# Kernel optimization log

Measured on AMD Instinct MI355X. Metric: run time of the kernel, lower is better.

The kernel has to match this reference:

```python
import jax, jax.numpy as jnp
import numpy as np

ALPHABET = 4
SKETCH_DIM = 128
SUBSEQ = 8
SEQ_LEN = 8192


def setup_inputs() -> dict:
    key = jax.random.key(0)
    k1, k2, k3 = jax.random.split(key, 3)
    sequence = jax.random.randint(k1, (SEQ_LEN,), 0, ALPHABET, dtype=jnp.int32)
    # stacked Linear(A, d, bias=False) weights, xavier-uniform-ish init
    limit = float(np.sqrt(6.0 / (ALPHABET + SKETCH_DIM)))
    hash_weights = jax.random.uniform(k2, (SUBSEQ, SKETCH_DIM, ALPHABET),
                                      minval=-limit, maxval=limit, dtype=jnp.float32)
    sign_weights = jax.random.normal(k3, (SUBSEQ, ALPHABET), dtype=jnp.float32)
    return {"sequence": sequence, "hash_weights": hash_weights, "sign_weights": sign_weights}


def _sketch(sequence, hash_weights, sign_weights):
    P, d, A = hash_weights.shape
    seq_len = sequence.shape[0]
    # circulant gather indices: roll(src, s)[j] == src[(j - s) % d]
    j = jnp.arange(d)
    idx = (j[:, None] - j[None, :]) % d  # [d(out), d(shift)]
    p_ids = jnp.arange(1, P + 1)
    z_num = p_ids.astype(jnp.float32)

    Tp0 = jnp.zeros((P + 1, d), jnp.float32).at[0, 0].set(1.0)
    Tm0 = jnp.zeros((P + 1, d), jnp.float32)

    def step(carry, xs):
        Tp, Tm = carry
        i, c = xs
        valid = (c >= 0) & (c < A)
        cc = jnp.clip(c, 0, A - 1)
        hv = hash_weights[:, :, cc]                      # [P, d]
        probs = jax.nn.softmax(hv, axis=1)               # [P, d]
        sign = jax.nn.sigmoid(sign_weights[:, cc])       # [P]
        denom = (i + 1).astype(jnp.float32)
        z = (z_num / denom)[:, None]                     # [P, 1]
        gate = ((p_ids <= i + 1) & valid)[:, None]       # [P, 1]
        # soft circular shift: sum_s probs[s] * roll(source, s)
        convP = jnp.einsum('pjs,ps->pj', Tp[:P][:, idx], probs)
        convM = jnp.einsum('pjs,ps->pj', Tm[:P][:, idx], probs)
        newP = jnp.where(gate, (1.0 - z) * Tp[1:] + z * sign[:, None] * convP, Tp[1:])
        newM = jnp.where(gate, (1.0 - z) * Tm[1:] + z * (1.0 - sign[:, None]) * convM, Tm[1:])
        return (Tp.at[1:].set(newP), Tm.at[1:].set(newM)), None

    (Tp, Tm), _ = jax.lax.scan(step, (Tp0, Tm0), (jnp.arange(seq_len), sequence))
    return Tp[P] - Tm[P]


def reference(sequence, hash_weights, sign_weights):
    return _sketch(sequence, hash_weights, sign_weights)
```

## Files before the change

kernel.cpp:

```cpp
#include <hip/hip_runtime.h>
#include <math.h>

#define DDIM 128
#define NSEQ 8192
#define SUB 16
#define SEG 64
#define NSEGB 128
#define COMB 16
#define NCOMB 8
#define NTRI 45

#define TRI(L,q) ((L)*((L)+1)/2 + (q))

#define OFF_PHAT 0
#define OFF_AB   32768
#define OFF_MSEG 557056
#define OFF_MG2  6455296

__device__ __forceinline__ void loadG(const float2* __restrict__ p, int fq,
                                      float (&R)[NTRI], float (&I)[NTRI]) {
#pragma unroll
  for (int e = 0; e < NTRI; ++e) {
    float2 t = p[e*128 + fq];
    R[e] = t.x; I[e] = t.y;
  }
}

__device__ __forceinline__ void matvec(const float (&GR)[NTRI], const float (&GI)[NTRI],
                                       float (&vr)[9], float (&vi)[9]) {
#pragma unroll
  for (int L = 8; L >= 0; --L) {
    float sr = 0.f, si = 0.f;
#pragma unroll
    for (int q = 0; q <= L; ++q) {
      float xr = vr[q], xi = vi[q];
      sr += GR[TRI(L,q)]*xr - GI[TRI(L,q)]*xi;
      si += GR[TRI(L,q)]*xi + GI[TRI(L,q)]*xr;
    }
    vr[L] = sr; vi[L] = si;
  }
}

__device__ __forceinline__ void matmul(const float (&BR)[NTRI], const float (&BI)[NTRI],
                                       float (&Ar)[NTRI], float (&Ai)[NTRI]) {
#pragma unroll
  for (int L = 8; L >= 0; --L) {
    float tr[9], ti[9];
#pragma unroll
    for (int q = 0; q <= L; ++q) {
      float sr = 0.f, si = 0.f;
#pragma unroll
      for (int r = q; r <= L; ++r) {
        float br = BR[TRI(L,r)], bi = BI[TRI(L,r)];
        float ar = Ar[TRI(r,q)], ai = Ai[TRI(r,q)];
        sr += br*ar - bi*ai;
        si += br*ai + bi*ar;
      }
      tr[q] = sr; ti[q] = si;
    }
#pragma unroll
    for (int q = 0; q <= L; ++q) { Ar[TRI(L,q)] = tr[q]; Ai[TRI(L,q)] = ti[q]; }
  }
}

__global__ __launch_bounds__(128)
void sk_setup(const int* __restrict__ seq,
              const float* __restrict__ hw,
              const float* __restrict__ sw,
              float2* __restrict__ phat,
              float2* __restrict__ ab)
{
  const int tid = threadIdx.x;
  const int bid = blockIdx.x;

  if (bid < 32) {
    __shared__ float probs[128];
    __shared__ float ct[128], st[128];
    __shared__ float red[4];
    const int r = bid, p = r >> 2, c = r & 3;
    const int wave = tid >> 6, lane = tid & 63;

    float h = hw[p*512 + tid*4 + c];
    float mx = h;
    #pragma unroll
    for (int off = 1; off < 64; off <<= 1) mx = fmaxf(mx, __shfl_xor(mx, off));
    if (lane == 0) red[wave] = mx;
    __syncthreads();
    mx = fmaxf(red[0], red[1]);
    float e = expf(h - mx);
    float s = e;
    #pragma unroll
    for (int off = 1; off < 64; off <<= 1) s += __shfl_xor(s, off);
    if (lane == 0) red[2 + wave] = s;
    float th = 6.28318530717958647692f * (float)tid / 128.0f;
    ct[tid] = cosf(th); st[tid] = sinf(th);
    __syncthreads();
    s = red[2] + red[3];
    probs[tid] = e / s;
    __syncthreads();

    float ar = 0.f, ai = 0.f;
    for (int j = 0; j < 128; ++j) {
      float pv = probs[j];
      int w = (j * tid) & 127;
      ar += pv * ct[w];
      ai -= pv * st[w];
    }
    phat[(c*8 + p)*128 + tid] = make_float2(ar, ai);
  } else {
    const int total = NSEQ * 8;
    for (int n = (bid - 32)*128 + tid; n < total; n += 64*128) {
      const int i = n >> 3, Lm1 = n & 7, L = Lm1 + 1;
      int cc0 = seq[i];
      bool valid = (cc0 >= 0) && (cc0 < 4);
      int cc = min(max(cc0, 0), 3);
      bool gate = valid && (L <= i + 1);
      float z  = (float)L / (float)(i + 1);
      float sg = 1.0f / (1.0f + expf(-sw[Lm1*4 + cc]));
      float a = gate ? (1.0f - z) : 1.0f;
      float b = gate ? (z * sg) : 0.0f;
      ab[n] = make_float2(a, b);
    }
  }
}

__global__ __launch_bounds__(512, 1)
void sk_seg(const int* __restrict__ seq,
            const float2* __restrict__ phat_g,
            const float2* __restrict__ ab_g,
            float2* __restrict__ mseg)
{
  __shared__ float2 phS[4096];
  __shared__ float2 abS[SEG*8];
  __shared__ int    chS[SEG];
  __shared__ float2 tb[2][NTRI*128];
  const int tid = threadIdx.x;
  const int u   = tid >> 7, fq = tid & 127;
  const int m   = blockIdx.x;

  {
    const float4* src = (const float4*)phat_g;
    float4* dst = (float4*)phS;
    for (int i = tid; i < 2048; i += 512) dst[i] = src[i];
  }
  for (int i = tid; i < SEG*8; i += 512) abS[i] = ab_g[m*SEG*8 + i];
  if (tid < SEG) chS[tid] = seq[m*SEG + tid];
  __syncthreads();

  float Mr[NTRI], Mi[NTRI];
  #pragma unroll
  for (int e = 0; e < NTRI; ++e) { Mr[e] = 0.f; Mi[e] = 0.f; }
  #pragma unroll
  for (int L = 0; L <= 8; ++L) Mr[TRI(L,L)] = 1.0f;

  const int t0 = u * SUB;
  for (int t = 0; t < SUB; ++t) {
    const int ts = t0 + t;
    const int c  = chS[ts];
    #pragma unroll
    for (int L = 8; L >= 1; --L) {
      float2 abv = abS[ts*8 + (L-1)];
      float2 Pv  = phS[(c*8 + (L-1))*128 + fq];
      const float a = abv.x;
      const float bPr = abv.y * Pv.x, bPi = abv.y * Pv.y;
      #pragma unroll
      for (int q = 0; q < L; ++q) {
        float xr = Mr[TRI(L-1,q)], xi = Mi[TRI(L-1,q)];
        Mr[TRI(L,q)] = a*Mr[TRI(L,q)] + (bPr*xr - bPi*xi);
        Mi[TRI(L,q)] = a*Mi[TRI(L,q)] + (bPr*xi + bPi*xr);
      }
      Mr[TRI(L,L)] *= a;
      Mi[TRI(L,L)] *= a;
    }
  }

  if (u == 1 || u == 3) {
    float2* b = tb[u >> 1];
    #pragma unroll
    for (int e = 0; e < NTRI; ++e) b[e*128 + fq] = make_float2(Mr[e], Mi[e]);
  }
  __syncthreads();
  if (u == 0 || u == 2) {
    const float2* b = tb[u >> 1];
    float Br[NTRI], Bi[NTRI];
    #pragma unroll
    for (int e = 0; e < NTRI; ++e) { float2 t = b[e*128 + fq]; Br[e] = t.x; Bi[e] = t.y; }
    matmul(Br, Bi, Mr, Mi);
  }
  __syncthreads();
  if (u == 2) {
    #pragma unroll
    for (int e = 0; e < NTRI; ++e) tb[1][e*128 + fq] = make_float2(Mr[e], Mi[e]);
  }
  __syncthreads();
  if (u == 0) {
    float Br[NTRI], Bi[NTRI];
    #pragma unroll
    for (int e = 0; e < NTRI; ++e) { float2 t = tb[1][e*128 + fq]; Br[e] = t.x; Bi[e] = t.y; }
    matmul(Br, Bi, Mr, Mi);
    #pragma unroll
    for (int e = 0; e < NTRI; ++e)
      mseg[((size_t)m*NTRI + e)*128 + fq] = make_float2(Mr[e], Mi[e]);
  }
}

__global__ __launch_bounds__(512, 1)
void sk_comb1(const float2* __restrict__ mseg, float2* __restrict__ mg2)
{
  __shared__ float2 tb[2][NTRI*128];
  const int tid = threadIdx.x;
  const int u   = tid >> 7, fq = tid & 127;
  const int g   = blockIdx.x;
  const float2* bp = mseg + (size_t)(g*COMB + u*4) * NTRI * 128;

  float Ar[NTRI], Ai[NTRI], Br[NTRI], Bi[NTRI];
  loadG(bp, fq, Ar, Ai);
  loadG(bp + (size_t)1*NTRI*128, fq, Br, Bi);  matmul(Br, Bi, Ar, Ai);
  loadG(bp + (size_t)2*NTRI*128, fq, Br, Bi);  matmul(Br, Bi, Ar, Ai);
  loadG(bp + (size_t)3*NTRI*128, fq, Br, Bi);  matmul(Br, Bi, Ar, Ai);

  if (u == 1 || u == 3) {
    float2* b = tb[u >> 1];
    #pragma unroll
    for (int e = 0; e < NTRI; ++e) b[e*128 + fq] = make_float2(Ar[e], Ai[e]);
  }
  __syncthreads();
  if (u == 0 || u == 2) {
    const float2* b = tb[u >> 1];
    #pragma unroll
    for (int e = 0; e < NTRI; ++e) { float2 t = b[e*128 + fq]; Br[e] = t.x; Bi[e] = t.y; }
    matmul(Br, Bi, Ar, Ai);
  }
  __syncthreads();
  if (u == 2) {
    #pragma unroll
    for (int e = 0; e < NTRI; ++e) tb[1][e*128 + fq] = make_float2(Ar[e], Ai[e]);
  }
  __syncthreads();
  if (u == 0) {
    #pragma unroll
    for (int e = 0; e < NTRI; ++e) { float2 t = tb[1][e*128 + fq]; Br[e] = t.x; Bi[e] = t.y; }
    matmul(Br, Bi, Ar, Ai);
    #pragma unroll
    for (int e = 0; e < NTRI; ++e)
      mg2[((size_t)g*NTRI + e)*128 + fq] = make_float2(Ar[e], Ai[e]);
  }
}

__global__ __launch_bounds__(512, 1)
void sk_fin(const float2* __restrict__ mg2, float* __restrict__ out)
{
  __shared__ float2 vS[9*128];
  __shared__ float Ur[128], Ui[128];
  __shared__ float ct[128], st[128];
  const int tid = threadIdx.x;
  const int u   = tid >> 7, fq = tid & 127;

  float Ar[NTRI], Ai[NTRI], Br[NTRI], Bi[NTRI];
  loadG(mg2 + (size_t)(2*u)  *NTRI*128, fq, Ar, Ai);
  loadG(mg2 + (size_t)(2*u+1)*NTRI*128, fq, Br, Bi);

  if (tid < 128) {
    float th = 6.28318530717958647692f * (float)tid / 128.0f;
    ct[tid] = cosf(th); st[tid] = sinf(th);
  }

  float vr[9], vi[9];
  if (u == 0) {
    #pragma unroll
    for (int L = 0; L <= 8; ++L) { vr[L] = Ar[TRI(L,0)]; vi[L] = Ai[TRI(L,0)]; }
    matvec(Br, Bi, vr, vi);
    #pragma unroll
    for (int L = 0; L <= 8; ++L) vS[L*128 + fq] = make_float2(vr[L], vi[L]);
  }
  __syncthreads();
  for (int uu = 1; uu < 4; ++uu) {
    if (u == uu) {
      #pragma unroll
      for (int L = 0; L <= 8; ++L) { float2 t = vS[L*128 + fq]; vr[L] = t.x; vi[L] = t.y; }
      matvec(Ar, Ai, vr, vi);
      matvec(Br, Bi, vr, vi);
      #pragma unroll
      for (int L = 0; L <= 8; ++L) vS[L*128 + fq] = make_float2(vr[L], vi[L]);
    }
    __syncthreads();
  }

  if (tid < 128) {
    float2 uv = vS[8*128 + tid];
    Ur[tid] = uv.x; Ui[tid] = uv.y;
  }
  __syncthreads();

  if (tid < 128) {
    float acc = 0.f;
    for (int k = 0; k < 128; ++k) {
      int w = (tid * k) & 127;
      acc += Ur[k]*ct[w] - Ui[k]*st[w];
    }
    out[tid] = acc * (1.0f/128.0f);
  }
}

extern "C" void kernel_launch(void* const* d_in, const int* in_sizes, int n_in,
                              void* d_out, int out_size, void* d_ws, size_t ws_size,
                              hipStream_t stream)
{
  const int*   seq = (const int*)d_in[0];
  const float* hw  = (const float*)d_in[1];
  const float* sw  = (const float*)d_in[2];

  char* base = (char*)d_ws;
  float2* phat = (float2*)(base + OFF_PHAT);
  float2* ab   = (float2*)(base + OFF_AB);
  float2* mseg = (float2*)(base + OFF_MSEG);
  float2* mg2  = (float2*)(base + OFF_MG2);

  sk_setup<<<96, 128, 0, stream>>>(seq, hw, sw, phat, ab);
  sk_seg<<<NSEGB, 512, 0, stream>>>(seq, phat, ab, mseg);
  sk_comb1<<<NCOMB, 512, 0, stream>>>(mseg, mg2);
  sk_fin<<<1, 512, 0, stream>>>(mg2, (float*)d_out);
}
```

Before: 140.0 us.

## Split segment combination into two parallel tree levels and widen final chain

```diff
diff --git a/kernel.cpp b/kernel.cpp
--- a/kernel.cpp
+++ b/kernel.cpp
@@ -6,8 +6,6 @@
 #define SUB 16
 #define SEG 64
 #define NSEGB 128
-#define COMB 16
-#define NCOMB 8
 #define NTRI 45
 
 #define TRI(L,q) ((L)*((L)+1)/2 + (q))
@@ -15,7 +13,8 @@
 #define OFF_PHAT 0
 #define OFF_AB   32768
 #define OFF_MSEG 557056
-#define OFF_MG2  6455296
+#define OFF_MT1  6455296
+#define OFF_MT2  7929856
 
 __device__ __forceinline__ void loadG(const float2* __restrict__ p, int fq,
                                       float (&R)[NTRI], float (&I)[NTRI]) {
@@ -24,6 +23,12 @@
     float2 t = p[e*128 + fq];
     R[e] = t.x; I[e] = t.y;
   }
+}
+
+__device__ __forceinline__ void publish(float2* __restrict__ b, int fq,
+                                        const float (&R)[NTRI], const float (&I)[NTRI]) {
+#pragma unroll
+  for (int e = 0; e < NTRI; ++e) b[e*128 + fq] = make_float2(R[e], I[e]);
 }
 
 __device__ __forceinline__ void matvec(const float (&GR)[NTRI], const float (&GI)[NTRI],
@@ -41,20 +46,25 @@
   }
 }
 
-__device__ __forceinline__ void matmul(const float (&BR)[NTRI], const float (&BI)[NTRI],
-                                       float (&Ar)[NTRI], float (&Ai)[NTRI]) {
+__device__ __forceinline__ void matmulL(const float2* __restrict__ b, int fq,
+                                        float (&Ar)[NTRI], float (&Ai)[NTRI]) {
 #pragma unroll
   for (int L = 8; L >= 0; --L) {
+    float Br_[9], Bi_[9];
+#pragma unroll
+    for (int r = 0; r <= L; ++r) {
+      float2 t = b[TRI(L,r)*128 + fq];
+      Br_[r] = t.x; Bi_[r] = t.y;
+    }
     float tr[9], ti[9];
 #pragma unroll
     for (int q = 0; q <= L; ++q) {
       float sr = 0.f, si = 0.f;
 #pragma unroll
       for (int r = q; r <= L; ++r) {
-        float br = BR[TRI(L,r)], bi = BI[TRI(L,r)];
         float ar = Ar[TRI(r,q)], ai = Ai[TRI(r,q)];
-        sr += br*ar - bi*ai;
-        si += br*ai + bi*ar;
+        sr += Br_[r]*ar - Bi_[r]*ai;
+        si += Br_[r]*ai + Bi_[r]*ar;
       }
       tr[q] = sr; ti[q] = si;
     }
@@ -124,7 +134,7 @@
   }
 }
 
-__global__ __launch_bounds__(512, 1)
+__global__ __launch_bounds__(512)
 void sk_seg(const int* __restrict__ seq,
             const float2* __restrict__ phat_g,
             const float2* __restrict__ ab_g,
@@ -174,81 +184,47 @@
     }
   }
 
-  if (u == 1 || u == 3) {
-    float2* b = tb[u >> 1];
-    #pragma unroll
-    for (int e = 0; e < NTRI; ++e) b[e*128 + fq] = make_float2(Mr[e], Mi[e]);
-  }
-  __syncthreads();
-  if (u == 0 || u == 2) {
-    const float2* b = tb[u >> 1];
-    float Br[NTRI], Bi[NTRI];
-    #pragma unroll
-    for (int e = 0; e < NTRI; ++e) { float2 t = b[e*128 + fq]; Br[e] = t.x; Bi[e] = t.y; }
-    matmul(Br, Bi, Mr, Mi);
-  }
-  __syncthreads();
-  if (u == 2) {
-    #pragma unroll
-    for (int e = 0; e < NTRI; ++e) tb[1][e*128 + fq] = make_float2(Mr[e], Mi[e]);
-  }
+  if (u == 1 || u == 3) publish(tb[u >> 1], fq, Mr, Mi);
+  __syncthreads();
+  if (u == 0 || u == 2) matmulL(tb[u >> 1], fq, Mr, Mi);
+  __syncthreads();
+  if (u == 2) publish(tb[1], fq, Mr, Mi);
   __syncthreads();
   if (u == 0) {
-    float Br[NTRI], Bi[NTRI];
-    #pragma unroll
-    for (int e = 0; e < NTRI; ++e) { float2 t = tb[1][e*128 + fq]; Br[e] = t.x; Bi[e] = t.y; }
-    matmul(Br, Bi, Mr, Mi);
+    matmulL(tb[1], fq, Mr, Mi);
     #pragma unroll
     for (int e = 0; e < NTRI; ++e)
       mseg[((size_t)m*NTRI + e)*128 + fq] = make_float2(Mr[e], Mi[e]);
   }
 }
 
-__global__ __launch_bounds__(512, 1)
-void sk_comb1(const float2* __restrict__ mseg, float2* __restrict__ mg2)
+__global__ __launch_bounds__(512)
+void sk_comb(const float2* __restrict__ min_, float2* __restrict__ mout)
 {
   __shared__ float2 tb[2][NTRI*128];
   const int tid = threadIdx.x;
   const int u   = tid >> 7, fq = tid & 127;
   const int g   = blockIdx.x;
-  const float2* bp = mseg + (size_t)(g*COMB + u*4) * NTRI * 128;
-
-  float Ar[NTRI], Ai[NTRI], Br[NTRI], Bi[NTRI];
-  loadG(bp, fq, Ar, Ai);
-  loadG(bp + (size_t)1*NTRI*128, fq, Br, Bi);  matmul(Br, Bi, Ar, Ai);
-  loadG(bp + (size_t)2*NTRI*128, fq, Br, Bi);  matmul(Br, Bi, Ar, Ai);
-  loadG(bp + (size_t)3*NTRI*128, fq, Br, Bi);  matmul(Br, Bi, Ar, Ai);
-
-  if (u == 1 || u == 3) {
-    float2* b = tb[u >> 1];
-    #pragma unroll
-    for (int e = 0; e < NTRI; ++e) b[e*128 + fq] = make_float2(Ar[e], Ai[e]);
-  }
-  __syncthreads();
-  if (u == 0 || u == 2) {
-    const float2* b = tb[u >> 1];
-    #pragma unroll
-    for (int e = 0; e < NTRI; ++e) { float2 t = b[e*128 + fq]; Br[e] = t.x; Bi[e] = t.y; }
-    matmul(Br, Bi, Ar, Ai);
-  }
-  __syncthreads();
-  if (u == 2) {
-    #pragma unroll
-    for (int e = 0; e < NTRI; ++e) tb[1][e*128 + fq] = make_float2(Ar[e], Ai[e]);
-  }
+
+  float Ar[NTRI], Ai[NTRI];
+  loadG(min_ + (size_t)(g*4 + u) * NTRI * 128, fq, Ar, Ai);
+
+  if (u == 1 || u == 3) publish(tb[u >> 1], fq, Ar, Ai);
+  __syncthreads();
+  if (u == 0 || u == 2) matmulL(tb[u >> 1], fq, Ar, Ai);
+  __syncthreads();
+  if (u == 2) publish(tb[1], fq, Ar, Ai);
   __syncthreads();
   if (u == 0) {
-    #pragma unroll
-    for (int e = 0; e < NTRI; ++e) { float2 t = tb[1][e*128 + fq]; Br[e] = t.x; Bi[e] = t.y; }
-    matmul(Br, Bi, Ar, Ai);
+    matmulL(tb[1], fq, Ar, Ai);
     #pragma unroll
     for (int e = 0; e < NTRI; ++e)
-      mg2[((size_t)g*NTRI + e)*128 + fq] = make_float2(Ar[e], Ai[e]);
-  }
-}
-
-__global__ __launch_bounds__(512, 1)
-void sk_fin(const float2* __restrict__ mg2, float* __restrict__ out)
+      mout[((size_t)g*NTRI + e)*128 + fq] = make_float2(Ar[e], Ai[e]);
+  }
+}
+
+__global__ __launch_bounds__(1024)
+void sk_fin(const float2* __restrict__ mg, float* __restrict__ out)
 {
   __shared__ float2 vS[9*128];
   __shared__ float Ur[128], Ui[128];
@@ -256,9 +232,8 @@
   const int tid = threadIdx.x;
   const int u   = tid >> 7, fq = tid & 127;
 
-  float Ar[NTRI], Ai[NTRI], Br[NTRI], Bi[NTRI];
-  loadG(mg2 + (size_t)(2*u)  *NTRI*128, fq, Ar, Ai);
-  loadG(mg2 + (size_t)(2*u+1)*NTRI*128, fq, Br, Bi);
+  float Ar[NTRI], Ai[NTRI];
+  loadG(mg + (size_t)u * NTRI * 128, fq, Ar, Ai);
 
   if (tid < 128) {
     float th = 6.28318530717958647692f * (float)tid / 128.0f;
@@ -269,17 +244,15 @@
   if (u == 0) {
     #pragma unroll
     for (int L = 0; L <= 8; ++L) { vr[L] = Ar[TRI(L,0)]; vi[L] = Ai[TRI(L,0)]; }
-    matvec(Br, Bi, vr, vi);
     #pragma unroll
     for (int L = 0; L <= 8; ++L) vS[L*128 + fq] = make_float2(vr[L], vi[L]);
   }
   __syncthreads();
-  for (int uu = 1; uu < 4; ++uu) {
+  for (int uu = 1; uu < 8; ++uu) {
     if (u == uu) {
       #pragma unroll
       for (int L = 0; L <= 8; ++L) { float2 t = vS[L*128 + fq]; vr[L] = t.x; vi[L] = t.y; }
       matvec(Ar, Ai, vr, vi);
-      matvec(Br, Bi, vr, vi);
       #pragma unroll
       for (int L = 0; L <= 8; ++L) vS[L*128 + fq] = make_float2(vr[L], vi[L]);
     }
@@ -314,10 +287,12 @@
   float2* phat = (float2*)(base + OFF_PHAT);
   float2* ab   = (float2*)(base + OFF_AB);
   float2* mseg = (float2*)(base + OFF_MSEG);
-  float2* mg2  = (float2*)(base + OFF_MG2);
+  float2* mt1  = (float2*)(base + OFF_MT1);
+  float2* mt2  = (float2*)(base + OFF_MT2);
 
   sk_setup<<<96, 128, 0, stream>>>(seq, hw, sw, phat, ab);
   sk_seg<<<NSEGB, 512, 0, stream>>>(seq, phat, ab, mseg);
-  sk_comb1<<<NCOMB, 512, 0, stream>>>(mseg, mg2);
-  sk_fin<<<1, 512, 0, stream>>>(mg2, (float*)d_out);
-}
+  sk_comb<<<32, 512, 0, stream>>>(mseg, mt1);
+  sk_comb<<<8, 512, 0, stream>>>(mt1, mt2);
+  sk_fin<<<1, 1024, 0, stream>>>(mt2, (float*)d_out);
+}
```

Measured after the change: 182.2 us. 1.3x slower.
